# Optimization experiments

Measured on AMD Instinct MI355X. Metric: run time of the kernel, lower is better.

## Reference

```python
import jax, jax.numpy as jnp
import numpy as np

IMG = 224  # hardcoded image resolution in the original module


def setup_inputs() -> dict:
    key = jax.random.key(0)
    ks = jax.random.split(key, 6)
    b, v, n, m = 16, 8, 8192, 1024
    pc = jax.random.normal(ks[0], (b, n, 3), jnp.float32)
    # binary silhouette masks (0/1 floats), ~half zeros so many outliers exist
    mask = (jax.random.uniform(ks[1], (b, v, IMG, IMG)) < 0.5).astype(jnp.float32)
    bounds = jax.random.uniform(ks[2], (b, v, m, 2), jnp.float32) * IMG
    inv_param = jax.random.normal(ks[3], (b, v, 4, 4), jnp.float32)
    proj_fine = jax.random.uniform(ks[4], (b, v, n, 2), jnp.float32) * IMG
    proj_finez = jax.random.uniform(ks[5], (b, v, n), jnp.float32) + 0.5
    return {"pc": pc, "mask": mask, "bounds": bounds, "inv_param": inv_param,
            "proj_fine": proj_fine, "proj_finez": proj_finez, "view_id": 3}


def reference(pc, mask, bounds, inv_param, proj_fine, proj_finez, view_id):
    b = pc.shape[0]
    # --- out_distance (only view_id affects the returned pc) ---
    pxy = proj_fine[:, view_id]                                  # (b, n, 2)
    pxy = jnp.stack([pxy[..., 0], IMG - pxy[..., 1]], axis=-1)   # flip y
    pxy_i = jnp.round(pxy).astype(jnp.int32)                     # round().long()
    # ZeroPad2d(1) then index with clamp(idx+1, 0, 225)
    mv = jnp.pad(mask[:, view_id], ((0, 0), (1, 1), (1, 1)))     # (b, 226, 226)
    xi = jnp.clip(pxy_i[..., 1] + 1, 0, IMG + 1)
    yi = jnp.clip(pxy_i[..., 0] + 1, 0, IMG + 1)
    bidx = jnp.arange(b)[:, None]
    out_mask = mv[bidx, xi, yi] == 0                             # (b, n) outliers
    # K=1 KNN of (rounded) outlier pixels against boundary points, both /224
    o = pxy_i.astype(bounds.dtype) / IMG                         # (b, n, 2)
    bd = bounds[:, view_id] / IMG                                # (b, m, 2)
    d2 = ((o * o).sum(-1)[:, :, None]
          + (bd * bd).sum(-1)[:, None, :]
          - 2.0 * jnp.einsum('bnd,bmd->bnm', o, bd))             # (b, n, m)
    nn_idx = jnp.argmin(d2, axis=-1)                             # (b, n)
    # n_bound * 224 == the original boundary point, gather directly
    n_bound = jnp.take_along_axis(bounds[:, view_id], nn_idx[:, :, None], axis=1)
    # --- move_out: back-project nearest boundary point, scatter into pc ---
    z = proj_finez[:, view_id][..., None]                        # (b, n, 1)
    hom = jnp.concatenate([n_bound * z, z, jnp.ones_like(z)], axis=-1)  # (b,n,4)
    back = jnp.einsum('bnk,bkl->bnl', hom, inv_param[:, view_id])[..., :3]
    return jnp.where(out_mask[..., None], back, pc)
```

## Files before the change

### kernel.cpp

```cpp
#include <hip/hip_runtime.h>
#include <math.h>

constexpr int IMG = 224;
constexpr int Bb  = 16;
constexpr int Vv  = 8;
constexpr int Nn  = 8192;
constexpr int Mm  = 1024;
constexpr int G   = 32;
constexpr float Hh = 1.0f / 32.0f;


__global__ __launch_bounds__(256) void prep_kernel(
    const float* __restrict__ bounds, const int* __restrict__ view_p,
    float4* __restrict__ ws_e, unsigned short* __restrict__ ws_s)
{
    const int view = *view_p;
    const int b = blockIdx.x;
    const int t = threadIdx.x;
    __shared__ int s_cnt[1024];
    __shared__ int s_cur[1024];
    __shared__ int s_part[256];
    #pragma unroll
    for (int u = 0; u < 4; ++u) s_cnt[t + 256 * u] = 0;
    __syncthreads();

    const float* bnd = bounds + (size_t)(b * Vv + view) * Mm * 2;
    float bdx[4], bdy[4];
    int cell[4];
    #pragma unroll
    for (int u = 0; u < 4; ++u) {
        int j = t + 256 * u;
        float2 bxy = reinterpret_cast<const float2*>(bnd)[j];
        bdx[u] = bxy.x / (float)IMG;
        bdy[u] = bxy.y / (float)IMG;
        int cx = min(G - 1, max(0, (int)(bdx[u] * (float)G)));
        int cy = min(G - 1, max(0, (int)(bdy[u] * (float)G)));
        cell[u] = cy * G + cx;
        atomicAdd(&s_cnt[cell[u]], 1);
    }
    __syncthreads();

    int c0 = s_cnt[4 * t], c1 = s_cnt[4 * t + 1];
    int c2 = s_cnt[4 * t + 2], c3 = s_cnt[4 * t + 3];
    int psum = c0 + c1 + c2 + c3;
    s_part[t] = psum;
    __syncthreads();
    for (int sh = 1; sh < 256; sh <<= 1) {
        int add = (t >= sh) ? s_part[t - sh] : 0;
        __syncthreads();
        s_part[t] += add;
        __syncthreads();
    }
    int base = s_part[t] - psum;
    int st0 = base, st1 = base + c0, st2 = base + c0 + c1, st3 = base + c0 + c1 + c2;
    unsigned short* wss = ws_s + b * 1040;
    wss[4 * t]     = (unsigned short)st0;
    wss[4 * t + 1] = (unsigned short)st1;
    wss[4 * t + 2] = (unsigned short)st2;
    wss[4 * t + 3] = (unsigned short)st3;
    if (t == 0) wss[1024] = (unsigned short)Mm;
    s_cur[4 * t] = st0; s_cur[4 * t + 1] = st1;
    s_cur[4 * t + 2] = st2; s_cur[4 * t + 3] = st3;
    __syncthreads();

    #pragma unroll
    for (int u = 0; u < 4; ++u) {
        int j = t + 256 * u;
        int pos = atomicAdd(&s_cur[cell[u]], 1);
        float nrm = __fadd_rn(__fmul_rn(bdx[u], bdx[u]), __fmul_rn(bdy[u], bdy[u]));
        ws_e[(size_t)b * Mm + pos] = make_float4(bdx[u], bdy[u], nrm, __int_as_float(j));
    }
}

__global__ __launch_bounds__(256, 8) void calib_kernel(
    const float* __restrict__ pc,
    const float* __restrict__ mask,
    const float* __restrict__ bounds,
    const float* __restrict__ inv_param,
    const float* __restrict__ proj_fine,
    const float* __restrict__ proj_finez,
    const int*   __restrict__ view_p,
    const float4* __restrict__ ws_e,
    const unsigned short* __restrict__ ws_s,
    float*       __restrict__ out)
{
    const int view = *view_p;
    const int b = blockIdx.y;
    const int t = threadIdx.x;
    const int s = t & 3;
    const int p = t >> 2;
    const int i = blockIdx.x * 64 + p;

    __shared__ float4 s_e[Mm];
    __shared__ unsigned short s_start[1032];
    const float4* we = ws_e + (size_t)b * Mm;
    #pragma unroll
    for (int u = 0; u < 4; ++u) s_e[t + 256 * u] = we[t + 256 * u];
    const unsigned short* wss = ws_s + b * 1040;
    for (int c = t; c < 1025; c += 256) s_start[c] = wss[c];
    __syncthreads();

    const size_t pf = (size_t)(b * Vv + view) * Nn + i;
    float2 pxy = reinterpret_cast<const float2*>(proj_fine)[pf];

    int i0 = (int)rintf(pxy.x);
    int i1 = (int)rintf((float)IMG - pxy.y);

    int xi = min(max(i1 + 1, 0), IMG + 1);
    int yi = min(max(i0 + 1, 0), IMG + 1);
    float mval = 0.0f;
    if (xi >= 1 && xi <= IMG && yi >= 1 && yi <= IMG)
        mval = mask[((size_t)(b * Vv + view) * IMG + (xi - 1)) * IMG + (yi - 1)];
    const bool use_back = (mval == 0.0f);

    if (use_back) {
        float ox = (float)i0 / (float)IMG;
        float oy = (float)i1 / (float)IMG;
        float o2 = __fadd_rn(__fmul_rn(ox, ox), __fmul_rn(oy, oy));
        float n2ox = __fmul_rn(-2.0f, ox);
        float n2oy = __fmul_rn(-2.0f, oy);

        int cx = min(G - 1, max(0, (int)(ox * (float)G)));
        int cy = min(G - 1, max(0, (int)(oy * (float)G)));

        float best = INFINITY;
        int   bj   = 0;

        int x0 = max(cx - 1, 0), x1 = min(cx + 1, G - 1);
        int b0 = 0, b1 = 0, b2 = 0, L0 = 0, L1 = 0, L2 = 0;
        if (cy - 1 >= 0) {
            int r = (cy - 1) * G;
            b0 = s_start[r + x0]; L0 = s_start[r + x1 + 1] - b0;
        }
        {
            int r = cy * G;
            b1 = s_start[r + x0]; L1 = s_start[r + x1 + 1] - b1;
        }
        if (cy + 1 < G) {
            int r = (cy + 1) * G;
            b2 = s_start[r + x0]; L2 = s_start[r + x1 + 1] - b2;
        }
        int L01 = L0 + L1;
        int T = L01 + L2;
        for (int u = s; u < T; u += 4) {
            bool inR1 = (u >= L0), inR2 = (u >= L01);
            int base = inR2 ? b2 : (inR1 ? b1 : b0);
            int off  = inR2 ? L01 : (inR1 ? L0 : 0);
            float4 cd = s_e[base + (u - off)];
            float dn = __fadd_rn(__fmul_rn(n2ox, cd.x), __fmul_rn(n2oy, cd.y));
            float d2 = __fadd_rn(__fadd_rn(o2, cd.z), dn);
            int   j  = __float_as_int(cd.w);
            bool better = (d2 < best) || (d2 == best && j < bj);
            best = better ? d2 : best;
            bj   = better ? j  : bj;
        }
        #pragma unroll
        for (int off = 1; off < 4; off <<= 1) {
            float bo = __shfl_xor(best, off);
            int   jo = __shfl_xor(bj, off);
            bool  c  = (bo < best) || (bo == best && jo < bj);
            best = c ? bo : best;
            bj   = c ? jo : bj;
        }

        if (!(best < Hh * Hh - 1e-5f)) {
            for (int k = s; k < 16; k += 4) {
                int xx, yy;
                if (k < 5)       { xx = cx - 2 + k;        yy = cy - 2; }
                else if (k < 10) { xx = cx - 2 + (k - 5);  yy = cy + 2; }
                else if (k < 13) { xx = cx - 2;            yy = cy - 1 + (k - 10); }
                else             { xx = cx + 2;            yy = cy - 1 + (k - 13); }
                if (xx >= 0 && xx < G && yy >= 0 && yy < G) {
                    int c = yy * G + xx;
                    int e0 = s_start[c], e1 = s_start[c + 1];
                    for (int e = e0; e < e1; ++e) {
                        float4 cd = s_e[e];
                        float dn = __fadd_rn(__fmul_rn(n2ox, cd.x), __fmul_rn(n2oy, cd.y));
                        float d2 = __fadd_rn(__fadd_rn(o2, cd.z), dn);
                        int   j  = __float_as_int(cd.w);
                        bool better = (d2 < best) || (d2 == best && j < bj);
                        best = better ? d2 : best;
                        bj   = better ? j  : bj;
                    }
                }
            }
            #pragma unroll
            for (int off = 1; off < 4; off <<= 1) {
                float bo = __shfl_xor(best, off);
                int   jo = __shfl_xor(bj, off);
                bool  c  = (bo < best) || (bo == best && jo < bj);
                best = c ? bo : best;
                bj   = c ? jo : bj;
            }

            if (!(best < 4.0f * Hh * Hh - 1e-5f) && s == 0) {
                for (int r = 3; r <= G; ++r) {
                    float lim = (float)(r - 1) * Hh;
                    if (best < lim * lim - 1e-5f) break;
                    int rx0 = max(0, cx - r), rx1 = min(G - 1, cx + r);
                    int ry0 = max(0, cy - r), ry1 = min(G - 1, cy + r);
                    for (int yy = ry0; yy <= ry1; ++yy) {
                        bool yedge = (yy == cy - r) || (yy == cy + r);
                        for (int xx = rx0; xx <= rx1; ++xx) {
                            if (!yedge && xx != cx - r && xx != cx + r) continue;
                            int c = yy * G + xx;
                            int e0 = s_start[c], e1 = s_start[c + 1];
                            for (int e = e0; e < e1; ++e) {
                                float4 cd = s_e[e];
                                float dn = __fadd_rn(__fmul_rn(n2ox, cd.x), __fmul_rn(n2oy, cd.y));
                                float d2 = __fadd_rn(__fadd_rn(o2, cd.z), dn);
                                int   j  = __float_as_int(cd.w);
                                bool better = (d2 < best) || (d2 == best && j < bj);
                                best = better ? d2 : best;
                                bj   = better ? j  : bj;
                            }
                        }
                    }
                }
            }
        }

        if (s == 0) {
            const float* bnd = bounds + (size_t)(b * Vv + view) * Mm * 2;
            float nbx = bnd[2 * bj];
            float nby = bnd[2 * bj + 1];
            float z   = proj_finez[pf];
            const float* ip = inv_param + (size_t)(b * Vv + view) * 16;
            float h0 = nbx * z, h1 = nby * z;
            float r0 = h0 * ip[0] + h1 * ip[4] + z * ip[8]  + ip[12];
            float r1 = h0 * ip[1] + h1 * ip[5] + z * ip[9]  + ip[13];
            float r2 = h0 * ip[2] + h1 * ip[6] + z * ip[10] + ip[14];
            const size_t ob = ((size_t)b * Nn + i) * 3;
            out[ob]     = r0;
            out[ob + 1] = r1;
            out[ob + 2] = r2;
        }
    } else if (s == 0) {
        const size_t ob = ((size_t)b * Nn + i) * 3;
        out[ob]     = pc[ob];
        out[ob + 1] = pc[ob + 1];
        out[ob + 2] = pc[ob + 2];
    }
}

__global__ __launch_bounds__(256) void calib_fallback(
    const float* __restrict__ pc, const float* __restrict__ mask,
    const float* __restrict__ bounds, const float* __restrict__ inv_param,
    const float* __restrict__ proj_fine, const float* __restrict__ proj_finez,
    const int* __restrict__ view_p, float* __restrict__ out)
{
    const int view = *view_p;
    const int b = blockIdx.y;
    const int s = threadIdx.x & 3;
    const int p_local = threadIdx.x >> 2;
    const int i = blockIdx.x * 64 + p_local;

    __shared__ float4 s_bd[Mm];
    const float* bnd = bounds + (size_t)(b * Vv + view) * Mm * 2;
    for (int j = threadIdx.x; j < Mm; j += 256) {
        float2 bxy = reinterpret_cast<const float2*>(bnd)[j];
        float bdx = bxy.x / (float)IMG;
        float bdy = bxy.y / (float)IMG;
        float nrm = __fadd_rn(__fmul_rn(bdx, bdx), __fmul_rn(bdy, bdy));
        s_bd[j] = make_float4(bdx, bdy, nrm, 0.0f);
    }
    __syncthreads();

    const size_t pf = (size_t)(b * Vv + view) * Nn + i;
    float2 pxy = reinterpret_cast<const float2*>(proj_fine)[pf];
    int i0 = (int)rintf(pxy.x);
    int i1 = (int)rintf((float)IMG - pxy.y);
    float ox = (float)i0 / (float)IMG;
    float oy = (float)i1 / (float)IMG;
    float o2 = __fadd_rn(__fmul_rn(ox, ox), __fmul_rn(oy, oy));
    float n2ox = __fmul_rn(-2.0f, ox);
    float n2oy = __fmul_rn(-2.0f, oy);

    float best = INFINITY;
    int bj = 0;
    const float4* sp = s_bd + s;
    #pragma unroll 4
    for (int q = 0; q < Mm / 4; ++q) {
        float4 bd = sp[4 * q];
        int j = 4 * q + s;
        float dn = __fadd_rn(__fmul_rn(n2ox, bd.x), __fmul_rn(n2oy, bd.y));
        float d2 = __fadd_rn(__fadd_rn(o2, bd.z), dn);
        bool c = d2 < best;
        bj = c ? j : bj;
        best = fminf(best, d2);
    }
    #pragma unroll
    for (int off = 1; off < 4; off <<= 1) {
        float bo = __shfl_xor(best, off);
        int   jo = __shfl_xor(bj, off);
        bool  c  = (bo < best) || (bo == best && jo < bj);
        best = c ? bo : best;
        bj   = c ? jo : bj;
    }
    if (s == 0) {
        int xi = min(max(i1 + 1, 0), IMG + 1);
        int yi = min(max(i0 + 1, 0), IMG + 1);
        float mval = 0.0f;
        if (xi >= 1 && xi <= IMG && yi >= 1 && yi <= IMG)
            mval = mask[((size_t)(b * Vv + view) * IMG + (xi - 1)) * IMG + (yi - 1)];
        const bool use_back = (mval == 0.0f);
        float nbx = bnd[2 * bj];
        float nby = bnd[2 * bj + 1];
        float z   = proj_finez[pf];
        const float* ip = inv_param + (size_t)(b * Vv + view) * 16;
        float h0 = nbx * z, h1 = nby * z;
        float r0 = h0 * ip[0] + h1 * ip[4] + z * ip[8]  + ip[12];
        float r1 = h0 * ip[1] + h1 * ip[5] + z * ip[9]  + ip[13];
        float r2 = h0 * ip[2] + h1 * ip[6] + z * ip[10] + ip[14];
        const size_t ob = ((size_t)b * Nn + i) * 3;
        float c0 = pc[ob], c1 = pc[ob + 1], c2 = pc[ob + 2];
        out[ob]     = use_back ? r0 : c0;
        out[ob + 1] = use_back ? r1 : c1;
        out[ob + 2] = use_back ? r2 : c2;
    }
}

extern "C" void kernel_launch(void* const* d_in, const int* in_sizes, int n_in,
                              void* d_out, int out_size, void* d_ws, size_t ws_size,
                              hipStream_t stream) {
    const float* pc         = (const float*)d_in[0];
    const float* mask       = (const float*)d_in[1];
    const float* bounds     = (const float*)d_in[2];
    const float* inv_param  = (const float*)d_in[3];
    const float* proj_fine  = (const float*)d_in[4];
    const float* proj_finez = (const float*)d_in[5];
    const int*   view_p     = (const int*)d_in[6];
    float* out = (float*)d_out;

    const size_t ws_need = (size_t)Bb * Mm * sizeof(float4)
                         + (size_t)Bb * 1040 * sizeof(unsigned short);
    if (ws_size >= ws_need) {
        float4* ws_e = (float4*)d_ws;
        unsigned short* ws_s =
            (unsigned short*)((char*)d_ws + (size_t)Bb * Mm * sizeof(float4));
        prep_kernel<<<dim3(Bb), 256, 0, stream>>>(bounds, view_p, ws_e, ws_s);
        dim3 grid(Nn / 64, Bb);
        calib_kernel<<<grid, 256, 0, stream>>>(pc, mask, bounds, inv_param,
                                               proj_fine, proj_finez, view_p,
                                               ws_e, ws_s, out);
    } else {
        dim3 grid(Nn / 64, Bb);
        calib_fallback<<<grid, 256, 0, stream>>>(pc, mask, bounds, inv_param,
                                                 proj_fine, proj_finez, view_p,
                                                 out);
    }
}
```

Measured before the change: 22.08 us.

## Search 5x5 cell window up front and use wavefront scan in prep

The prep kernel's block-wide Hillis-Steele prefix sum over shared memory is replaced by a wavefront shuffle scan plus a small per-wave total array, which cuts many barriers and frees the s_cur/s_part buffers. The calib kernel now scans the full 5x5 neighbourhood of grid cells in one flattened, lane-strided loop instead of a 3x3 pass followed by a conditional ring-2 pass. This removes a divergent second phase and an extra shuffle reduction, at the cost of always visiting about 25/9 as many candidate points per outlier, even when the 3x3 result would already have been final.

```diff
diff --git a/kernel.cpp b/kernel.cpp
--- a/kernel.cpp
+++ b/kernel.cpp
@@ -17,9 +17,10 @@
     const int view = *view_p;
     const int b = blockIdx.x;
     const int t = threadIdx.x;
+    const int lane = t & 63;
+    const int w = t >> 6;
     __shared__ int s_cnt[1024];
-    __shared__ int s_cur[1024];
-    __shared__ int s_part[256];
+    __shared__ int s_wtot[4];
     #pragma unroll
     for (int u = 0; u < 4; ++u) s_cnt[t + 256 * u] = 0;
     __syncthreads();
@@ -43,15 +44,17 @@
     int c0 = s_cnt[4 * t], c1 = s_cnt[4 * t + 1];
     int c2 = s_cnt[4 * t + 2], c3 = s_cnt[4 * t + 3];
     int psum = c0 + c1 + c2 + c3;
-    s_part[t] = psum;
-    __syncthreads();
-    for (int sh = 1; sh < 256; sh <<= 1) {
-        int add = (t >= sh) ? s_part[t - sh] : 0;
-        __syncthreads();
-        s_part[t] += add;
-        __syncthreads();
-    }
-    int base = s_part[t] - psum;
+    int incl = psum;
+    #pragma unroll
+    for (int off = 1; off < 64; off <<= 1) {
+        int v = __shfl_up(incl, off);
+        if (lane >= off) incl += v;
+    }
+    if (lane == 63) s_wtot[w] = incl;
+    __syncthreads();
+    int basew = 0;
+    for (int ww = 0; ww < w; ++ww) basew += s_wtot[ww];
+    int base = basew + incl - psum;
     int st0 = base, st1 = base + c0, st2 = base + c0 + c1, st3 = base + c0 + c1 + c2;
     unsigned short* wss = ws_s + b * 1040;
     wss[4 * t]     = (unsigned short)st0;
@@ -59,14 +62,14 @@
     wss[4 * t + 2] = (unsigned short)st2;
     wss[4 * t + 3] = (unsigned short)st3;
     if (t == 0) wss[1024] = (unsigned short)Mm;
-    s_cur[4 * t] = st0; s_cur[4 * t + 1] = st1;
-    s_cur[4 * t + 2] = st2; s_cur[4 * t + 3] = st3;
+    s_cnt[4 * t] = st0; s_cnt[4 * t + 1] = st1;
+    s_cnt[4 * t + 2] = st2; s_cnt[4 * t + 3] = st3;
     __syncthreads();
 
     #pragma unroll
     for (int u = 0; u < 4; ++u) {
         int j = t + 256 * u;
-        int pos = atomicAdd(&s_cur[cell[u]], 1);
+        int pos = atomicAdd(&s_cnt[cell[u]], 1);
         float nrm = __fadd_rn(__fmul_rn(bdx[u], bdx[u]), __fmul_rn(bdy[u], bdy[u]));
         ws_e[(size_t)b * Mm + pos] = make_float4(bdx[u], bdy[u], nrm, __int_as_float(j));
     }
@@ -126,26 +129,28 @@
         float best = INFINITY;
         int   bj   = 0;
 
-        int x0 = max(cx - 1, 0), x1 = min(cx + 1, G - 1);
-        int b0 = 0, b1 = 0, b2 = 0, L0 = 0, L1 = 0, L2 = 0;
-        if (cy - 1 >= 0) {
-            int r = (cy - 1) * G;
-            b0 = s_start[r + x0]; L0 = s_start[r + x1 + 1] - b0;
-        }
-        {
-            int r = cy * G;
-            b1 = s_start[r + x0]; L1 = s_start[r + x1 + 1] - b1;
-        }
-        if (cy + 1 < G) {
-            int r = (cy + 1) * G;
-            b2 = s_start[r + x0]; L2 = s_start[r + x1 + 1] - b2;
-        }
-        int L01 = L0 + L1;
-        int T = L01 + L2;
+        int x0 = max(cx - 2, 0), x1 = min(cx + 2, G - 1);
+        int bases[5], offs[5];
+        int T = 0;
+        #pragma unroll
+        for (int r = 0; r < 5; ++r) {
+            int yy = cy - 2 + r;
+            int bb = 0, LL = 0;
+            if (yy >= 0 && yy < G) {
+                int rowb = yy * G;
+                bb = s_start[rowb + x0];
+                LL = s_start[rowb + x1 + 1] - bb;
+            }
+            bases[r] = bb; offs[r] = T; T += LL;
+        }
         for (int u = s; u < T; u += 4) {
-            bool inR1 = (u >= L0), inR2 = (u >= L01);
-            int base = inR2 ? b2 : (inR1 ? b1 : b0);
-            int off  = inR2 ? L01 : (inR1 ? L0 : 0);
+            int base = bases[0], off = offs[0];
+            #pragma unroll
+            for (int r = 1; r < 5; ++r) {
+                bool in = (u >= offs[r]);
+                base = in ? bases[r] : base;
+                off  = in ? offs[r]  : off;
+            }
             float4 cd = s_e[base + (u - off)];
             float dn = __fadd_rn(__fmul_rn(n2ox, cd.x), __fmul_rn(n2oy, cd.y));
             float d2 = __fadd_rn(__fadd_rn(o2, cd.z), dn);
@@ -163,57 +168,26 @@
             bj   = c ? jo : bj;
         }
 
-        if (!(best < Hh * Hh - 1e-5f)) {
-            for (int k = s; k < 16; k += 4) {
-                int xx, yy;
-                if (k < 5)       { xx = cx - 2 + k;        yy = cy - 2; }
-                else if (k < 10) { xx = cx - 2 + (k - 5);  yy = cy + 2; }
-                else if (k < 13) { xx = cx - 2;            yy = cy - 1 + (k - 10); }
-                else             { xx = cx + 2;            yy = cy - 1 + (k - 13); }
-                if (xx >= 0 && xx < G && yy >= 0 && yy < G) {
-                    int c = yy * G + xx;
-                    int e0 = s_start[c], e1 = s_start[c + 1];
-                    for (int e = e0; e < e1; ++e) {
-                        float4 cd = s_e[e];
-                        float dn = __fadd_rn(__fmul_rn(n2ox, cd.x), __fmul_rn(n2oy, cd.y));
-                        float d2 = __fadd_rn(__fadd_rn(o2, cd.z), dn);
-                        int   j  = __float_as_int(cd.w);
-                        bool better = (d2 < best) || (d2 == best && j < bj);
-                        best = better ? d2 : best;
-                        bj   = better ? j  : bj;
-                    }
-                }
-            }
-            #pragma unroll
-            for (int off = 1; off < 4; off <<= 1) {
-                float bo = __shfl_xor(best, off);
-                int   jo = __shfl_xor(bj, off);
-                bool  c  = (bo < best) || (bo == best && jo < bj);
-                best = c ? bo : best;
-                bj   = c ? jo : bj;
-            }
-
-            if (!(best < 4.0f * Hh * Hh - 1e-5f) && s == 0) {
-                for (int r = 3; r <= G; ++r) {
-                    float lim = (float)(r - 1) * Hh;
-                    if (best < lim * lim - 1e-5f) break;
-                    int rx0 = max(0, cx - r), rx1 = min(G - 1, cx + r);
-                    int ry0 = max(0, cy - r), ry1 = min(G - 1, cy + r);
-                    for (int yy = ry0; yy <= ry1; ++yy) {
-                        bool yedge = (yy == cy - r) || (yy == cy + r);
-                        for (int xx = rx0; xx <= rx1; ++xx) {
-                            if (!yedge && xx != cx - r && xx != cx + r) continue;
-                            int c = yy * G + xx;
-                            int e0 = s_start[c], e1 = s_start[c + 1];
-                            for (int e = e0; e < e1; ++e) {
-                                float4 cd = s_e[e];
-                                float dn = __fadd_rn(__fmul_rn(n2ox, cd.x), __fmul_rn(n2oy, cd.y));
-                                float d2 = __fadd_rn(__fadd_rn(o2, cd.z), dn);
-                                int   j  = __float_as_int(cd.w);
-                                bool better = (d2 < best) || (d2 == best && j < bj);
-                                best = better ? d2 : best;
-                                bj   = better ? j  : bj;
-                            }
+        if (!(best < 4.0f * Hh * Hh - 1e-5f) && s == 0) {
+            for (int r = 3; r <= G; ++r) {
+                float lim = (float)(r - 1) * Hh;
+                if (best < lim * lim - 1e-5f) break;
+                int rx0 = max(0, cx - r), rx1 = min(G - 1, cx + r);
+                int ry0 = max(0, cy - r), ry1 = min(G - 1, cy + r);
+                for (int yy = ry0; yy <= ry1; ++yy) {
+                    bool yedge = (yy == cy - r) || (yy == cy + r);
+                    for (int xx = rx0; xx <= rx1; ++xx) {
+                        if (!yedge && xx != cx - r && xx != cx + r) continue;
+                        int c = yy * G + xx;
+                        int e0 = s_start[c], e1 = s_start[c + 1];
+                        for (int e = e0; e < e1; ++e) {
+                            float4 cd = s_e[e];
+                            float dn = __fadd_rn(__fmul_rn(n2ox, cd.x), __fmul_rn(n2oy, cd.y));
+                            float d2 = __fadd_rn(__fadd_rn(o2, cd.z), dn);
+                            int   j  = __float_as_int(cd.w);
+                            bool better = (d2 < best) || (d2 == best && j < bj);
+                            best = better ? d2 : best;
+                            bj   = better ? j  : bj;
                         }
                     }
                 }
```

After: 21.31 us. -3.5%, faster.
